# Kernel optimization log

Hardware: AMD Instinct MI355X
Metric: run time of the kernel (lower is better)

## Reference

```python
import jax, jax.numpy as jnp
import numpy as np

B, S, D = 4, 2048, 1024
H, HD = 16, 64  # n_head, head_dim; H*HD == D

def setup_inputs() -> dict:
    key = jax.random.key(0)
    k1, k2, k3 = jax.random.split(key, 3)
    x = jax.random.normal(k1, (B, S, D), dtype=jnp.float32)
    # nn.Linear weights: stored [out, in]; init ~ U(-1/sqrt(in), 1/sqrt(in))
    w_attn = jax.random.uniform(k2, (3 * D, D), dtype=jnp.float32,
                                minval=-1.0, maxval=1.0) / jnp.sqrt(jnp.float32(D))
    w_proj = jax.random.uniform(k3, (D, D), dtype=jnp.float32,
                                minval=-1.0, maxval=1.0) / jnp.sqrt(jnp.float32(D))
    return {"x": x, "w_attn": w_attn, "w_proj": w_proj}

def reference(x, w_attn, w_proj):
    b, s, d = x.shape
    qkv = jnp.einsum('bsd,ed->bse', x, w_attn)              # [b, s, 3D]
    q, k, v = jnp.split(qkv, 3, axis=-1)
    q = q.reshape(b, s, H, HD).transpose(0, 2, 1, 3)        # [b, h, s, hd]
    k = k.reshape(b, s, H, HD).transpose(0, 2, 1, 3)
    v = v.reshape(b, s, H, HD).transpose(0, 2, 1, 3)
    scale = 1.0 / jnp.sqrt(jnp.float32(HD))
    scores = jnp.einsum('bhqd,bhkd->bhqk', q, k) * scale    # [b, h, s, s]
    causal = jnp.tril(jnp.ones((s, s), dtype=bool))
    scores = jnp.where(causal[None, None], scores, -jnp.inf)
    attn = jax.nn.softmax(scores, axis=-1)
    out = jnp.einsum('bhqk,bhkd->bhqd', attn, v)            # [b, h, s, hd]
    out = out.transpose(0, 2, 1, 3).reshape(b, s, d)
    return jnp.einsum('bsd,ed->bse', out, w_proj)
```

## Files before the change

kernel.cpp:

```cpp
#include <hip/hip_runtime.h>
#include <hip/hip_bf16.h>

#define NB   4
#define SEQ  2048
#define DMODEL 1024
#define NHEAD 16
#define HDIM 64
#define MROWS (NB * SEQ)
#define N_QKV (3 * DMODEL)

typedef __attribute__((ext_vector_type(8))) short bf16x8;
typedef __attribute__((ext_vector_type(4))) float f32x4;

#define MFMA16(a, b, c) __builtin_amdgcn_mfma_f32_16x16x32_bf16((a), (b), (c), 0, 0, 0)

__device__ inline bf16x8 load16(const __hip_bfloat16* p) {
    union { uint4 u; bf16x8 v; } t;
    t.u = *(const uint4*)p;
    return t.v;
}

__device__ inline ushort f2bf(float f) {
    union { float f; unsigned int u; } a;
    a.f = f;
    unsigned int r = a.u + 0x7FFFu + ((a.u >> 16) & 1u);
    return (ushort)(r >> 16);
}

__device__ inline unsigned int cvt_pk_bf16(float lo, float hi) {
    unsigned int r;
    asm("v_cvt_pk_bf16_f32 %0, %1, %2" : "=v"(r) : "v"(lo), "v"(hi));
    return r;
}

__device__ inline void gload_lds16(const __hip_bfloat16* g, __hip_bfloat16* l) {
    __builtin_amdgcn_global_load_lds(
        (const __attribute__((address_space(1))) unsigned int*)g,
        (__attribute__((address_space(3))) unsigned int*)l,
        16, 0, 0);
}

__global__ __launch_bounds__(256)
void cast_bf16_kernel(const float* __restrict__ in, ushort* __restrict__ out, int n,
                      int scale_n, float sc) {
    int idx = (blockIdx.x * 256 + threadIdx.x) * 4;
    if (idx + 3 < n) {
        float4 v = *(const float4*)(in + idx);
        float s = (idx < scale_n) ? sc : 1.0f;
        ushort4 o;
        o.x = f2bf(v.x * s);
        o.y = f2bf(v.y * s);
        o.z = f2bf(v.z * s);
        o.w = f2bf(v.w * s);
        *(ushort4*)(out + idx) = o;
    }
}

template<int MODE>
__global__ __launch_bounds__(256)
void gemm_bt(const __hip_bfloat16* __restrict__ A,
             const __hip_bfloat16* __restrict__ Bm,
             ushort* __restrict__ Cb,
             float* __restrict__ Cf,
             ushort* __restrict__ Vt,
             int M, int N, int K) {
    constexpr int BM = 128, BN = 128, BK = 32, LDT = 32;
    __shared__ __hip_bfloat16 As[BM * LDT];
    __shared__ __hip_bfloat16 Bs[BN * LDT];

    const int tid  = threadIdx.x;
    const int lane = tid & 63;
    const int wave = tid >> 6;
    const int wr = (wave >> 1) * 64;
    const int wc = (wave & 1) * 64;
    const int quad = lane >> 4;
    const int l16  = lane & 15;

    const int row0 = blockIdx.y * BM;
    const int col0 = blockIdx.x * BN;

    const int srow = lane >> 2;
    const int scol = (lane & 3) * 8;

    f32x4 acc[4][4];
#pragma unroll
    for (int i = 0; i < 4; i++)
#pragma unroll
        for (int j = 0; j < 4; j++) acc[i][j] = (f32x4)0.0f;

    for (int k0 = 0; k0 < K; k0 += BK) {
#pragma unroll
        for (int c = 0; c < 2; c++) {
            const int seg = wave * 2 + c;
            const int r = seg * 16 + srow;
            gload_lds16(A  + (size_t)(row0 + r) * K + k0 + scol, As + seg * 512);
            gload_lds16(Bm + (size_t)(col0 + r) * K + k0 + scol, Bs + seg * 512);
        }
        __syncthreads();

        bf16x8 af[4], bfr[4];
#pragma unroll
        for (int t = 0; t < 4; t++) {
            af[t]  = load16(&As[(wr + t * 16 + l16) * LDT + quad * 8]);
            bfr[t] = load16(&Bs[(wc + t * 16 + l16) * LDT + quad * 8]);
        }
#pragma unroll
        for (int i = 0; i < 4; i++)
#pragma unroll
            for (int j = 0; j < 4; j++)
                acc[i][j] = MFMA16(af[i], bfr[j], acc[i][j]);
        __syncthreads();
    }

    if constexpr (MODE == 2) {
        if (col0 >= 2 * DMODEL) {
            __shared__ ushort Ts[64 * 136];
            const int vcol0 = col0 - 2 * DMODEL;
            const int bb = row0 >> 11;
            const int row0m = row0 & 2047;
#pragma unroll
            for (int half = 0; half < 2; half++) {
                if ((wave & 1) == half) {
#pragma unroll
                    for (int i = 0; i < 4; i++)
#pragma unroll
                        for (int j = 0; j < 4; j++) {
                            int c = j * 16 + l16;
                            int rb = wr + i * 16 + quad * 4;
#pragma unroll
                            for (int r = 0; r < 4; r++)
                                Ts[c * 136 + rb + r] = f2bf(acc[i][j][r]);
                        }
                }
                __syncthreads();
                int col = tid >> 2, part = tid & 3;
                int hh = (vcol0 >> 6) + half;
                ushort* dp = Vt + (((size_t)(bb * NHEAD + hh)) * HDIM + col) * SEQ
                                + row0m + part * 32;
                const ushort* sp = &Ts[col * 136 + part * 32];
#pragma unroll
                for (int k = 0; k < 4; k++)
                    *(uint4*)(dp + k * 8) = *(const uint4*)(sp + k * 8);
                __syncthreads();
            }
            return;
        }
    }

    ushort* base = nullptr;
    int c0 = 0;
    if constexpr (MODE == 2) {
        base = Cb + ((col0 >= DMODEL) ? (size_t)MROWS * DMODEL : 0);
        c0 = col0 & (DMODEL - 1);
    }
#pragma unroll
    for (int i = 0; i < 4; i++) {
#pragma unroll
        for (int r = 0; r < 4; r++) {
            size_t grow = (size_t)(row0 + wr + i * 16 + quad * 4 + r);
#pragma unroll
            for (int j = 0; j < 4; j++) {
                float v = acc[i][j][r];
                if (MODE == 1) {
                    Cf[grow * N + col0 + wc + j * 16 + l16] = v;
                } else {
                    base[grow * DMODEL + c0 + wc + j * 16 + l16] = f2bf(v);
                }
            }
        }
    }
}

__global__ __launch_bounds__(256)
void attn_kernel(const ushort* __restrict__ Qb, const ushort* __restrict__ Kb,
                 const ushort* __restrict__ Vtb, ushort* __restrict__ O) {
    constexpr int LDP = 40;
    __shared__ __hip_bfloat16 Kc[3 * 32 * 64];
    __shared__ __hip_bfloat16 Vc[3 * 64 * 32];
    __shared__ ushort Pld[4 * 16 * LDP];

    const int tid  = threadIdx.x;
    const int wave = tid >> 6;
    const int lane = tid & 63;
    const int quad = lane >> 4;
    const int l16  = lane & 15;

    const int blk = (int)blockIdx.x;
    const int g   = 15 - (blk >> 6);
    const int bh  = (((blk >> 3) & 7) << 3) | (blk & 7);
    const int b = bh >> 4, h = bh & 15;
    const int p  = 4 * g + wave;
    const int q0 = p * 32;
    const int nc = p + 1;
    const int ncmax = 4 * g + 4;

    bf16x8 ones;
#pragma unroll
    for (int i = 0; i < 8; i++) ones[i] = (short)0x3F80;

    bf16x8 qf[2][2];
#pragma unroll
    for (int s = 0; s < 2; s++) {
        const __hip_bfloat16* qp = (const __hip_bfloat16*)Qb
            + ((size_t)b * SEQ + q0 + s * 16 + l16) * DMODEL + h * HDIM;
        qf[s][0] = load16(qp + quad * 8);
        qf[s][1] = load16(qp + 32 + quad * 8);
    }

    const __hip_bfloat16* kbase = (const __hip_bfloat16*)Kb + (size_t)b * SEQ * DMODEL + h * HDIM;
    const __hip_bfloat16* vbase = (const __hip_bfloat16*)Vtb + (size_t)bh * HDIM * SEQ;

    f32x4 oacc[2][4], lacc[2];
#pragma unroll
    for (int s = 0; s < 2; s++) {
        lacc[s] = (f32x4)0.0f;
#pragma unroll
        for (int t = 0; t < 4; t++) oacc[s][t] = (f32x4)0.0f;
    }

    ushort* myP = Pld + wave * (16 * LDP);

    const int slot = wave * 64 + lane;
    const int skey = slot >> 3;
    const int sdsg = (slot & 7) ^ (skey & 7);
    const int svd  = slot >> 2;
    const int svsg = slot & 3;
    const __hip_bfloat16* kg = kbase + (size_t)skey * DMODEL + sdsg * 8;
    const __hip_bfloat16* vg = vbase + (size_t)svd * SEQ + svsg * 8;

    auto stage = [&](int buf) {
        gload_lds16(kg, Kc + buf * 2048 + wave * 512);
        gload_lds16(vg, Vc + buf * 2048 + wave * 512);
        kg += 32 * DMODEL;
        vg += 32;
    };

    stage(0);
    stage(1);
    asm volatile("s_waitcnt vmcnt(2)" ::: "memory");
    __builtin_amdgcn_s_barrier();
    asm volatile("" ::: "memory");

    for (int c = 0; c < ncmax; ++c) {
        const int cur = c % 3;
        const bool more = (c + 2 < ncmax);
        if (more) stage((c + 2) % 3);

        if (c < nc) {
            const int k0 = c * 32;
            const bool diag = (c == nc - 1);
            const __hip_bfloat16* Kb_l = Kc + cur * 2048;
            const __hip_bfloat16* Vb_l = Vc + cur * 2048;

            bf16x8 kb[2][2], vb[4];
#pragma unroll
            for (int t = 0; t < 2; t++) {
#pragma unroll
                for (int hf = 0; hf < 2; hf++)
                    kb[t][hf] = load16(&Kb_l[(t * 16 + l16) * 64
                                             + (((hf * 4 + quad) ^ (l16 & 7)) * 8)]);
            }
#pragma unroll
            for (int t = 0; t < 4; t++)
                vb[t] = load16(&Vb_l[(t * 16 + l16) * 32 + quad * 8]);

#pragma unroll
            for (int s = 0; s < 2; s++) {
                f32x4 z[2];
#pragma unroll
                for (int t = 0; t < 2; t++) {
                    f32x4 zz = (f32x4)0.0f;
                    zz = MFMA16(kb[t][0], qf[s][0], zz);
                    zz = MFMA16(kb[t][1], qf[s][1], zz);
                    z[t] = zz;
                }

#pragma unroll
                for (int t = 0; t < 2; t++) {
                    float e[4];
#pragma unroll
                    for (int r = 0; r < 4; r++) {
                        float sv = z[t][r];
                        if (diag) {
                            int key = k0 + t * 16 + quad * 4 + r;
                            int qq  = q0 + s * 16 + l16;
                            sv = (key <= qq) ? sv : -1e30f;
                        }
                        e[r] = __builtin_amdgcn_exp2f(sv);
                    }
                    uint2 w;
                    w.x = cvt_pk_bf16(e[0], e[1]);
                    w.y = cvt_pk_bf16(e[2], e[3]);
                    *(uint2*)&myP[l16 * LDP + t * 16 + quad * 4] = w;
                }
                bf16x8 pa = load16((const __hip_bfloat16*)&myP[l16 * LDP + quad * 8]);

#pragma unroll
                for (int t = 0; t < 4; t++)
                    oacc[s][t] = MFMA16(pa, vb[t], oacc[s][t]);
                lacc[s] = MFMA16(pa, ones, lacc[s]);
            }
        }

        if (more) asm volatile("s_waitcnt vmcnt(2)" ::: "memory");
        else      asm volatile("s_waitcnt vmcnt(0)" ::: "memory");
        __builtin_amdgcn_s_barrier();
        asm volatile("" ::: "memory");
    }

#pragma unroll
    for (int s = 0; s < 2; s++) {
        float inv[4];
#pragma unroll
        for (int r = 0; r < 4; r++) inv[r] = 1.0f / lacc[s][r];
#pragma unroll
        for (int t = 0; t < 4; t++) {
#pragma unroll
            for (int r = 0; r < 4; r++) {
                float v = oacc[s][t][r] * inv[r];
                O[((size_t)b * SEQ + q0 + s * 16 + quad * 4 + r) * DMODEL
                  + h * HDIM + t * 16 + l16] = f2bf(v);
            }
        }
    }
}

extern "C" void kernel_launch(void* const* d_in, const int* in_sizes, int n_in,
                              void* d_out, int out_size, void* d_ws, size_t ws_size,
                              hipStream_t stream) {
    const float* x      = (const float*)d_in[0];
    const float* w_attn = (const float*)d_in[1];
    const float* w_proj = (const float*)d_in[2];
    float* out = (float*)d_out;

    ushort* ws   = (ushort*)d_ws;
    ushort* xb   = ws;
    ushort* wab  = xb  + (size_t)MROWS * DMODEL;
    ushort* wpb  = wab + (size_t)N_QKV * DMODEL;
    ushort* qkvb = wpb + (size_t)DMODEL * DMODEL;
    ushort* ob   = qkvb + (size_t)MROWS * N_QKV;

    ushort* qreg = qkvb;
    ushort* kreg = qkvb + (size_t)MROWS * DMODEL;
    ushort* vtreg = qkvb + 2 * (size_t)MROWS * DMODEL;

    const int n_x  = MROWS * DMODEL;
    const int n_wa = N_QKV * DMODEL;
    const int n_wp = DMODEL * DMODEL;

    const float qsc = 0.125f * 1.44269504f;

    cast_bf16_kernel<<<n_x / 1024, 256, 0, stream>>>(x, xb, n_x, 0, 1.0f);
    cast_bf16_kernel<<<n_wa / 1024, 256, 0, stream>>>(w_attn, wab, n_wa,
                                                      DMODEL * DMODEL, qsc);
    cast_bf16_kernel<<<n_wp / 1024, 256, 0, stream>>>(w_proj, wpb, n_wp, 0, 1.0f);

    gemm_bt<2><<<dim3(N_QKV / 128, MROWS / 128), 256, 0, stream>>>(
        (const __hip_bfloat16*)xb, (const __hip_bfloat16*)wab, qreg, nullptr, vtreg,
        MROWS, N_QKV, DMODEL);

    attn_kernel<<<1024, 256, 0, stream>>>(qreg, kreg, vtreg, ob);

    gemm_bt<1><<<dim3(DMODEL / 128, MROWS / 128), 256, 0, stream>>>(
        (const __hip_bfloat16*)ob, (const __hip_bfloat16*)wpb, nullptr, out, nullptr,
        MROWS, DMODEL, DMODEL);
}
```

Before: 281.5 us.

## Triple-buffer GEMM LDS loads with 256x128 tiles, swizzle and block remap

Reworks the bf16 GEMM into 512-thread blocks with 256x128 tiles and a three-stage LDS ring. Global-to-LDS loads are issued two iterations ahead and waited on with vmcnt counters plus a single barrier per step. It also XOR-swizzles the LDS layout to avoid bank conflicts, remaps block indices for L2 locality, raises wave priority around the MFMAs, and rewrites the V-transpose epilogue to use per-wave scratch without block barriers. The aim is to hide global load latency and cut synchronisation overhead. The cost is more LDS per block and fewer blocks in the grid.

```diff
diff --git a/kernel.cpp b/kernel.cpp
--- a/kernel.cpp
+++ b/kernel.cpp
@@ -57,30 +57,46 @@
 }
 
 template<int MODE>
-__global__ __launch_bounds__(256)
+__global__ __launch_bounds__(512, 4)
 void gemm_bt(const __hip_bfloat16* __restrict__ A,
              const __hip_bfloat16* __restrict__ Bm,
              ushort* __restrict__ Cb,
              float* __restrict__ Cf,
              ushort* __restrict__ Vt,
              int M, int N, int K) {
-    constexpr int BM = 128, BN = 128, BK = 32, LDT = 32;
-    __shared__ __hip_bfloat16 As[BM * LDT];
-    __shared__ __hip_bfloat16 Bs[BN * LDT];
+    constexpr int BM = 256, BN = 128, BK = 32;
+    __shared__ __hip_bfloat16 As[3 * BM * BK];
+    __shared__ __hip_bfloat16 Bs[3 * BN * BK];
 
     const int tid  = threadIdx.x;
+    const int wave = tid >> 6;
     const int lane = tid & 63;
-    const int wave = tid >> 6;
+    const int quad = lane >> 4;
+    const int l16  = lane & 15;
     const int wr = (wave >> 1) * 64;
     const int wc = (wave & 1) * 64;
-    const int quad = lane >> 4;
-    const int l16  = lane & 15;
-
-    const int row0 = blockIdx.y * BM;
-    const int col0 = blockIdx.x * BN;
-
-    const int srow = lane >> 2;
-    const int scol = (lane & 3) * 8;
+
+    const int nbx  = gridDim.x;
+    const int nblk = nbx * gridDim.y;
+    const int orig = (int)blockIdx.y * nbx + (int)blockIdx.x;
+    const int swzb = (orig & 7) * (nblk >> 3) + (orig >> 3);
+    const int bx = swzb % nbx, by = swzb / nbx;
+
+    const int row0 = by * BM;
+    const int col0 = bx * BN;
+
+    const int srow = tid >> 2;
+    const int ssl  = ((tid & 3) ^ ((tid >> 3) & 3)) * 8;
+    const __hip_bfloat16* ag0 = A  + (size_t)(row0 +       srow) * K + ssl;
+    const __hip_bfloat16* ag1 = A  + (size_t)(row0 + 128 + srow) * K + ssl;
+    const __hip_bfloat16* bg0 = Bm + (size_t)(col0 +       srow) * K + ssl;
+
+    auto stage = [&](int buf) {
+        gload_lds16(ag0, As + buf * (BM * BK) + wave * 512);
+        gload_lds16(ag1, As + buf * (BM * BK) + 4096 + wave * 512);
+        gload_lds16(bg0, Bs + buf * (BN * BK) + wave * 512);
+        ag0 += BK; ag1 += BK; bg0 += BK;
+    };
 
     f32x4 acc[4][4];
 #pragma unroll
@@ -88,60 +104,67 @@
 #pragma unroll
         for (int j = 0; j < 4; j++) acc[i][j] = (f32x4)0.0f;
 
-    for (int k0 = 0; k0 < K; k0 += BK) {
-#pragma unroll
-        for (int c = 0; c < 2; c++) {
-            const int seg = wave * 2 + c;
-            const int r = seg * 16 + srow;
-            gload_lds16(A  + (size_t)(row0 + r) * K + k0 + scol, As + seg * 512);
-            gload_lds16(Bm + (size_t)(col0 + r) * K + k0 + scol, Bs + seg * 512);
-        }
-        __syncthreads();
-
+    stage(0);
+    stage(1);
+    asm volatile("s_waitcnt vmcnt(3)" ::: "memory");
+    __builtin_amdgcn_s_barrier();
+    asm volatile("" ::: "memory");
+
+    const int nk = K / BK;
+    const int swzr = (l16 >> 1) & 3;
+    for (int t = 0; t < nk; ++t) {
+        const int cur = t % 3;
+        const bool more = (t + 2 < nk);
+        if (more) stage((t + 2) % 3);
+
+        const __hip_bfloat16* Ab = As + cur * (BM * BK);
+        const __hip_bfloat16* Bb = Bs + cur * (BN * BK);
         bf16x8 af[4], bfr[4];
 #pragma unroll
-        for (int t = 0; t < 4; t++) {
-            af[t]  = load16(&As[(wr + t * 16 + l16) * LDT + quad * 8]);
-            bfr[t] = load16(&Bs[(wc + t * 16 + l16) * LDT + quad * 8]);
-        }
+        for (int i = 0; i < 4; i++) {
+            af[i]  = load16(&Ab[(wr + i * 16 + l16) * 32 + ((quad ^ swzr) * 8)]);
+            bfr[i] = load16(&Bb[(wc + i * 16 + l16) * 32 + ((quad ^ swzr) * 8)]);
+        }
+
+        __builtin_amdgcn_s_setprio(1);
 #pragma unroll
         for (int i = 0; i < 4; i++)
 #pragma unroll
             for (int j = 0; j < 4; j++)
                 acc[i][j] = MFMA16(af[i], bfr[j], acc[i][j]);
-        __syncthreads();
+        __builtin_amdgcn_s_setprio(0);
+
+        if (more) asm volatile("s_waitcnt vmcnt(3)" ::: "memory");
+        else      asm volatile("s_waitcnt vmcnt(0)" ::: "memory");
+        __builtin_amdgcn_s_barrier();
+        asm volatile("" ::: "memory");
     }
 
     if constexpr (MODE == 2) {
         if (col0 >= 2 * DMODEL) {
-            __shared__ ushort Ts[64 * 136];
             const int vcol0 = col0 - 2 * DMODEL;
             const int bb = row0 >> 11;
             const int row0m = row0 & 2047;
-#pragma unroll
-            for (int half = 0; half < 2; half++) {
-                if ((wave & 1) == half) {
-#pragma unroll
-                    for (int i = 0; i < 4; i++)
-#pragma unroll
-                        for (int j = 0; j < 4; j++) {
-                            int c = j * 16 + l16;
-                            int rb = wr + i * 16 + quad * 4;
-#pragma unroll
-                            for (int r = 0; r < 4; r++)
-                                Ts[c * 136 + rb + r] = f2bf(acc[i][j][r]);
-                        }
+            const int hh = (vcol0 >> 6) + (wave & 1);
+            ushort* Tw = (ushort*)As + wave * 2048;
+            ushort* vdst = Vt + ((size_t)(bb * NHEAD + hh) * HDIM) * SEQ;
+#pragma unroll
+            for (int P = 0; P < 2; P++) {
+#pragma unroll
+                for (int i2 = 0; i2 < 2; i2++)
+#pragma unroll
+                    for (int j = 0; j < 4; j++)
+#pragma unroll
+                        for (int r = 0; r < 4; r++)
+                            Tw[(j * 16 + l16) * 32 + i2 * 16 + quad * 4 + r] =
+                                f2bf(acc[2 * P + i2][j][r]);
+#pragma unroll
+                for (int pp = 0; pp < 4; pp++) {
+                    int d = pp * 16 + (lane >> 2);
+                    int part = lane & 3;
+                    uint4 v = *(const uint4*)(Tw + d * 32 + part * 8);
+                    *(uint4*)(vdst + (size_t)d * SEQ + row0m + wr + P * 32 + part * 8) = v;
                 }
-                __syncthreads();
-                int col = tid >> 2, part = tid & 3;
-                int hh = (vcol0 >> 6) + half;
-                ushort* dp = Vt + (((size_t)(bb * NHEAD + hh)) * HDIM + col) * SEQ
-                                + row0m + part * 32;
-                const ushort* sp = &Ts[col * 136 + part * 32];
-#pragma unroll
-                for (int k = 0; k < 4; k++)
-                    *(uint4*)(dp + k * 8) = *(const uint4*)(sp + k * 8);
-                __syncthreads();
             }
             return;
         }
@@ -355,13 +378,13 @@
                                                       DMODEL * DMODEL, qsc);
     cast_bf16_kernel<<<n_wp / 1024, 256, 0, stream>>>(w_proj, wpb, n_wp, 0, 1.0f);
 
-    gemm_bt<2><<<dim3(N_QKV / 128, MROWS / 128), 256, 0, stream>>>(
+    gemm_bt<2><<<dim3(N_QKV / 128, MROWS / 256), 512, 0, stream>>>(
         (const __hip_bfloat16*)xb, (const __hip_bfloat16*)wab, qreg, nullptr, vtreg,
         MROWS, N_QKV, DMODEL);
 
     attn_kernel<<<1024, 256, 0, stream>>>(qreg, kreg, vtreg, ob);
 
-    gemm_bt<1><<<dim3(DMODEL / 128, MROWS / 128), 256, 0, stream>>>(
+    gemm_bt<1><<<dim3(DMODEL / 128, MROWS / 256), 512, 0, stream>>>(
         (const __hip_bfloat16*)ob, (const __hip_bfloat16*)wpb, nullptr, out, nullptr,
         MROWS, DMODEL, DMODEL);
 }
```

After: 269.2 us. 1.05x faster.
